# Kernel tuning notes

Measured on AMD Instinct MI355X. Metric: run time of the kernel, lower is better.

The kernel has to match this reference:

```python
import jax, jax.numpy as jnp
import numpy as np


def setup_inputs() -> dict:
    key = jax.random.key(0)
    k1, k2 = jax.random.split(key)
    batch, n = 1024, 32768
    x = jax.random.normal(k1, (batch, 1, n), dtype=jnp.float32)
    activ = jax.random.uniform(k2, (1, n), dtype=jnp.float32)  # EMA buffer state (nonnegative like mean(|x|))
    std = jnp.ones((1,), dtype=jnp.float32)
    return {"x": x, "activ": activ, "std": std}


def reference(x, activ, std):
    batch = x.shape[0]
    # EMA buffer update: activ = 0.97*activ + 0.03*mean(|x|, axis=0)
    activ_new = 0.97 * activ + 0.03 * jnp.mean(jnp.abs(x), axis=0)  # [1, n]
    ac = jnp.exp(-5.0 * jnp.squeeze(activ_new))                      # [n]
    s = jnp.sum(ac)
    ac = ac.at[0].set(s * 4000.0)  # heavily weight index 0 (the "no perturbation" slot)
    # torch.multinomial(ac, batch, replacement=True) == categorical with logits=log(weights)
    r = jax.random.categorical(jax.random.key(42), jnp.log(ac), shape=(batch,))  # [batch] in [0, n)
    i = jnp.arange(batch)
    # x[i, 0, r] += std * (r > 0); (i, r_i) pairs are unique per row so scatter-add == indexed add
    x = x.at[i, 0, r].add(std * (r > 0).astype(x.dtype))
    return x
```

## Files before the change

kernel.cpp:

```cpp
#include <hip/hip_runtime.h>
#include <math.h>

#define NROWS 1024
#define NCOLS 32768
#define NC4   (NCOLS / 4)
#define KCAND 16
#define TH_BITS 0xFFFC0000u
#define T_GUARD 7.9e-5f

__device__ __forceinline__ void tf_round(unsigned &x0, unsigned &x1, int r) {
    x0 += x1;
    x1 = __builtin_rotateleft32(x1, r);
    x1 ^= x0;
}

__device__ __forceinline__ void threefry2x32_key0_42(unsigned &x0, unsigned &x1) {
    const unsigned k0 = 0u;
    const unsigned k1 = 42u;
    const unsigned k2 = 0x1BD11BDAu ^ k0 ^ k1;
    x0 += k0; x1 += k1;
    tf_round(x0, x1, 13); tf_round(x0, x1, 15); tf_round(x0, x1, 26); tf_round(x0, x1, 6);
    x0 += k1; x1 += k2 + 1u;
    tf_round(x0, x1, 17); tf_round(x0, x1, 29); tf_round(x0, x1, 16); tf_round(x0, x1, 24);
    x0 += k2; x1 += k0 + 2u;
    tf_round(x0, x1, 13); tf_round(x0, x1, 15); tf_round(x0, x1, 26); tf_round(x0, x1, 6);
    x0 += k0; x1 += k1 + 3u;
    tf_round(x0, x1, 17); tf_round(x0, x1, 29); tf_round(x0, x1, 16); tf_round(x0, x1, 24);
    x0 += k1; x1 += k2 + 4u;
    tf_round(x0, x1, 13); tf_round(x0, x1, 15); tf_round(x0, x1, 26); tf_round(x0, x1, 6);
    x0 += k2; x1 += k0 + 5u;
}

__device__ __forceinline__ float bits_to_u(unsigned bits) {
    float u = __uint_as_float((bits >> 9) | 0x3f800000u) - 1.0f;
    return fmaxf(u, 1.17549435e-38f);
}

__global__ __launch_bounds__(256) void kF(
        const float4* __restrict__ x4, float4* __restrict__ out4,
        float4* __restrict__ partial4, unsigned* __restrict__ bits0,
        unsigned* __restrict__ cnt, uint2* __restrict__ cand, int nrb) {
    const int b = blockIdx.x;
    const int t = threadIdx.x;
    const int rpb = NROWS / nrb;

    auto copy_part = [&]() {
        if (b >= nrb * 32) return;
        const int bx = b & 31, by = b >> 5;
        const int j4 = bx * 256 + t;
        size_t base = (size_t)(by * rpb) * NC4 + j4;
        float4 acc = make_float4(0.f, 0.f, 0.f, 0.f);
        #pragma unroll 8
        for (int r = 0; r < rpb; ++r) {
            float4 v = x4[base];
            out4[base] = v;
            acc.x += fabsf(v.x); acc.y += fabsf(v.y);
            acc.z += fabsf(v.z); acc.w += fabsf(v.w);
            base += NC4;
        }
        partial4[(size_t)by * NC4 + j4] = acc;
    };

    auto scan_part = [&]() {
        const unsigned cbase = (unsigned)b * (unsigned)NCOLS;
        #pragma unroll 2
        for (int i = 0; i < NCOLS / 256; ++i) {
            const int j = t + (i << 8);
            unsigned x0 = 0u, x1 = cbase + (unsigned)j;
            threefry2x32_key0_42(x0, x1);
            const unsigned bits = x0 ^ x1;
            if (j == 0) {
                bits0[b] = bits;
            } else if (bits >= TH_BITS) {
                unsigned pos = atomicAdd(&cnt[b], 1u);
                if (pos < KCAND) cand[b * KCAND + pos] = make_uint2((unsigned)j, bits);
            }
        }
    };

    if (b & 1) { scan_part(); copy_part(); }
    else       { copy_part(); scan_part(); }
}

__global__ __launch_bounds__(256) void k2_weights(
        const float* __restrict__ partial, const float* __restrict__ activ,
        float* __restrict__ w, float* __restrict__ blocksums,
        float* __restrict__ blockmins, int nrb) {
    const int t = threadIdx.x;
    const int j = blockIdx.x * 256 + t;
    float s = 0.f;
    for (int rb = 0; rb < nrb; ++rb) s += partial[rb * NCOLS + j];
    float m  = s * (1.0f / (float)NROWS);
    float a  = 0.97f * activ[j] + 0.03f * m;
    float ac = expf(-5.0f * a);
    float wj = 1.0f / ac;
    w[j] = wj;
    __shared__ float reds[256];
    __shared__ float redm[256];
    reds[t] = ac;
    redm[t] = (j == 0) ? INFINITY : wj;
    __syncthreads();
    for (int off = 128; off > 0; off >>= 1) {
        if (t < off) {
            reds[t] += reds[t + off];
            redm[t] = fminf(redm[t], redm[t + off]);
        }
        __syncthreads();
    }
    if (t == 0) { blocksums[blockIdx.x] = reds[0]; blockmins[blockIdx.x] = redm[0]; }
}

__global__ __launch_bounds__(128) void k3_scalars(
        const float* __restrict__ blocksums, const float* __restrict__ blockmins,
        float* __restrict__ w, float* __restrict__ wminp) {
    const int t = threadIdx.x;
    __shared__ float reds[128];
    __shared__ float redm[128];
    reds[t] = blocksums[t];
    redm[t] = blockmins[t];
    __syncthreads();
    for (int off = 64; off > 0; off >>= 1) {
        if (t < off) {
            reds[t] += reds[t + off];
            redm[t] = fminf(redm[t], redm[t + off]);
        }
        __syncthreads();
    }
    if (t == 0) { w[0] = 1.0f / (reds[0] * 4000.0f); wminp[0] = redm[0]; }
}

__global__ __launch_bounds__(64) void k4b_resolve(
        const float* __restrict__ w, const unsigned* __restrict__ bits0,
        const unsigned* __restrict__ cnt, const uint2* __restrict__ cand,
        const float* __restrict__ wminp, const float* __restrict__ stdp,
        float* __restrict__ out) {
    const int r = blockIdx.x;
    const int t = threadIdx.x;
    const float w0   = w[0];
    const float wmin = wminp[0];
    const float val0 = -__log2f(bits_to_u(bits0[r])) * w0;
    const unsigned c = cnt[r];
    const bool slow = (c > KCAND) || !(val0 < T_GUARD * wmin);

    if (!slow) {
        if (t == 0 && c > 0) {
            float best = INFINITY;
            int   bi   = 0x7FFFFFFF;
            for (int k = 0; k < (int)c; ++k) {
                uint2 cd = cand[r * KCAND + k];
                float v = -__log2f(bits_to_u(cd.y)) * w[cd.x];
                int   j = (int)cd.x;
                if (v < best || (v == best && j < bi)) { best = v; bi = j; }
            }
            if (best < val0 && bi > 0 && bi < NCOLS)
                out[(size_t)r * NCOLS + bi] += stdp[0];
        }
        return;
    }

    const unsigned cbase = (unsigned)r * (unsigned)NCOLS;
    float best = INFINITY;
    int   bi   = 0x7FFFFFFF;
    for (int j = t; j < NCOLS; j += 64) {
        if (j == 0) continue;
        unsigned x0 = 0u, x1 = cbase + (unsigned)j;
        threefry2x32_key0_42(x0, x1);
        float v = -__log2f(bits_to_u(x0 ^ x1)) * w[j];
        if (v < best) { best = v; bi = j; }
    }
    __shared__ float sv[64];
    __shared__ int   si[64];
    sv[t] = best; si[t] = bi;
    __syncthreads();
    for (int off = 32; off > 0; off >>= 1) {
        if (t < off) {
            float ov = sv[t + off]; int oi = si[t + off];
            if (ov < sv[t] || (ov == sv[t] && oi < si[t])) { sv[t] = ov; si[t] = oi; }
        }
        __syncthreads();
    }
    if (t == 0) {
        if (sv[0] < val0 && si[0] > 0 && si[0] < NCOLS)
            out[(size_t)r * NCOLS + si[0]] += stdp[0];
    }
}

extern "C" void kernel_launch(void* const* d_in, const int* in_sizes, int n_in,
                              void* d_out, int out_size, void* d_ws, size_t ws_size,
                              hipStream_t stream) {
    (void)in_sizes; (void)n_in; (void)out_size;
    const float* x     = (const float*)d_in[0];
    const float* activ = (const float*)d_in[1];
    const float* stdp  = (const float*)d_in[2];
    float* out = (float*)d_out;
    char*  ws  = (char*)d_ws;

    const size_t tail_bytes = (size_t)NCOLS * 4 + 128 * 4 + 128 * 4 + 4
                            + NROWS * 4 + NROWS * 4 + (size_t)NROWS * KCAND * 8;
    int nrb = 16;
    if (ws_size >= (size_t)32 * NCOLS * 4 + tail_bytes) nrb = 32;

    float*    partial   = (float*)ws;
    float*    wbuf      = (float*)(ws + (size_t)nrb * NCOLS * 4);
    float*    blocksums = wbuf + NCOLS;
    float*    blockmins = blocksums + 128;
    float*    wminp     = blockmins + 128;
    unsigned* bits0     = (unsigned*)(wminp + 1);
    unsigned* cnt       = bits0 + NROWS;
    uint2*    cand      = (uint2*)(cnt + NROWS);

    hipMemsetAsync(cnt, 0, NROWS * sizeof(unsigned), stream);
    kF<<<NROWS, 256, 0, stream>>>((const float4*)x, (float4*)out,
                                  (float4*)partial, bits0, cnt, cand, nrb);
    k2_weights<<<NCOLS / 256, 256, 0, stream>>>(partial, activ, wbuf,
                                                blocksums, blockmins, nrb);
    k3_scalars<<<1, 128, 0, stream>>>(blocksums, blockmins, wbuf, wminp);
    k4b_resolve<<<NROWS, 64, 0, stream>>>(wbuf, bits0, cnt, cand, wminp,
                                          stdp, out);
}
```

Measured before the change: 303.0 us.

## Split copy and RNG scan into separate interleaved blocks; fold scalar reduction into resolve

The fused kernel no longer runs a copy and a full-row RNG scan in every block. Copy blocks are now interleaved with dedicated scan blocks, and each scan block covers half a row, giving 2048 scan blocks. The output copy uses nontemporal stores, and the candidate counters are zeroed inside the kernel, which removes the memset. The separate scalar-reduction kernel is dropped and its reduction is redone redundantly in each resolve block. This cuts two launches and should balance memory-bound and ALU-bound work across CUs, at the cost of extra redundant reductions and more total blocks.

```diff
diff --git a/kernel.cpp b/kernel.cpp
--- a/kernel.cpp
+++ b/kernel.cpp
@@ -4,9 +4,13 @@
 #define NROWS 1024
 #define NCOLS 32768
 #define NC4   (NCOLS / 4)
+#define HCOLS (NCOLS / 2)
+#define NB_SCAN 2048
 #define KCAND 16
 #define TH_BITS 0xFFFC0000u
 #define T_GUARD 7.9e-5f
+
+typedef float vfloat4 __attribute__((ext_vector_type(4)));
 
 __device__ __forceinline__ void tf_round(unsigned &x0, unsigned &x1, int r) {
     x0 += x1;
@@ -39,47 +43,49 @@
 __global__ __launch_bounds__(256) void kF(
         const float4* __restrict__ x4, float4* __restrict__ out4,
         float4* __restrict__ partial4, unsigned* __restrict__ bits0,
-        unsigned* __restrict__ cnt, uint2* __restrict__ cand, int nrb) {
+        unsigned* __restrict__ cnt, uint2* __restrict__ cand,
+        int nrb, int stride) {
     const int b = blockIdx.x;
     const int t = threadIdx.x;
-    const int rpb = NROWS / nrb;
-
-    auto copy_part = [&]() {
-        if (b >= nrb * 32) return;
-        const int bx = b & 31, by = b >> 5;
+
+    if (b % stride == 0) {
+        const int cid = b / stride;
+        const int rpb = NROWS / nrb;
+        const int bx = cid & 31, by = cid >> 5;
         const int j4 = bx * 256 + t;
         size_t base = (size_t)(by * rpb) * NC4 + j4;
         float4 acc = make_float4(0.f, 0.f, 0.f, 0.f);
         #pragma unroll 8
         for (int r = 0; r < rpb; ++r) {
             float4 v = x4[base];
-            out4[base] = v;
+            vfloat4 nv = { v.x, v.y, v.z, v.w };
+            __builtin_nontemporal_store(nv, (vfloat4*)&out4[base]);
             acc.x += fabsf(v.x); acc.y += fabsf(v.y);
             acc.z += fabsf(v.z); acc.w += fabsf(v.w);
             base += NC4;
         }
         partial4[(size_t)by * NC4 + j4] = acc;
-    };
-
-    auto scan_part = [&]() {
-        const unsigned cbase = (unsigned)b * (unsigned)NCOLS;
+    } else {
+        const int sid = b - b / stride - 1;
+        const int row = sid >> 1, half = sid & 1;
+        if (t == 0) cnt[sid] = 0;
+        __syncthreads();
+        const unsigned cbase = (unsigned)row * (unsigned)NCOLS;
+        const int jbase = half * HCOLS;
         #pragma unroll 2
-        for (int i = 0; i < NCOLS / 256; ++i) {
-            const int j = t + (i << 8);
+        for (int i = 0; i < HCOLS / 256; ++i) {
+            const int j = jbase + (i << 8) + t;
             unsigned x0 = 0u, x1 = cbase + (unsigned)j;
             threefry2x32_key0_42(x0, x1);
             const unsigned bits = x0 ^ x1;
             if (j == 0) {
-                bits0[b] = bits;
+                bits0[row] = bits;
             } else if (bits >= TH_BITS) {
-                unsigned pos = atomicAdd(&cnt[b], 1u);
-                if (pos < KCAND) cand[b * KCAND + pos] = make_uint2((unsigned)j, bits);
+                unsigned pos = atomicAdd(&cnt[sid], 1u);
+                if (pos < KCAND) cand[sid * KCAND + pos] = make_uint2((unsigned)j, bits);
             }
         }
-    };
-
-    if (b & 1) { scan_part(); copy_part(); }
-    else       { copy_part(); scan_part(); }
+    }
 }
 
 __global__ __launch_bounds__(256) void k2_weights(
@@ -110,44 +116,47 @@
     if (t == 0) { blocksums[blockIdx.x] = reds[0]; blockmins[blockIdx.x] = redm[0]; }
 }
 
-__global__ __launch_bounds__(128) void k3_scalars(
-        const float* __restrict__ blocksums, const float* __restrict__ blockmins,
-        float* __restrict__ w, float* __restrict__ wminp) {
-    const int t = threadIdx.x;
-    __shared__ float reds[128];
-    __shared__ float redm[128];
-    reds[t] = blocksums[t];
-    redm[t] = blockmins[t];
-    __syncthreads();
-    for (int off = 64; off > 0; off >>= 1) {
-        if (t < off) {
-            reds[t] += reds[t + off];
-            redm[t] = fminf(redm[t], redm[t + off]);
-        }
-        __syncthreads();
-    }
-    if (t == 0) { w[0] = 1.0f / (reds[0] * 4000.0f); wminp[0] = redm[0]; }
-}
-
-__global__ __launch_bounds__(64) void k4b_resolve(
-        const float* __restrict__ w, const unsigned* __restrict__ bits0,
+__global__ __launch_bounds__(64) void k4_resolve(
+        const float* __restrict__ w, const float* __restrict__ blocksums,
+        const float* __restrict__ blockmins, const unsigned* __restrict__ bits0,
         const unsigned* __restrict__ cnt, const uint2* __restrict__ cand,
-        const float* __restrict__ wminp, const float* __restrict__ stdp,
-        float* __restrict__ out) {
+        const float* __restrict__ stdp, float* __restrict__ out) {
     const int r = blockIdx.x;
     const int t = threadIdx.x;
-    const float w0   = w[0];
-    const float wmin = wminp[0];
+    __shared__ float sv[64];
+    __shared__ float sm[64];
+    __shared__ int   si[64];
+
+    sv[t] = blocksums[t] + blocksums[t + 64];
+    sm[t] = fminf(blockmins[t], blockmins[t + 64]);
+    __syncthreads();
+    for (int off = 32; off > 0; off >>= 1) {
+        if (t < off) {
+            sv[t] += sv[t + off];
+            sm[t] = fminf(sm[t], sm[t + off]);
+        }
+        __syncthreads();
+    }
+    const float w0   = 1.0f / (sv[0] * 4000.0f);
+    const float wmin = sm[0];
+
     const float val0 = -__log2f(bits_to_u(bits0[r])) * w0;
-    const unsigned c = cnt[r];
-    const bool slow = (c > KCAND) || !(val0 < T_GUARD * wmin);
+    const unsigned c0 = cnt[2 * r];
+    const unsigned c1 = cnt[2 * r + 1];
+    const bool slow = (c0 > KCAND) || (c1 > KCAND) || !(val0 < T_GUARD * wmin);
 
     if (!slow) {
-        if (t == 0 && c > 0) {
+        if (t == 0 && (c0 | c1) != 0u) {
             float best = INFINITY;
             int   bi   = 0x7FFFFFFF;
-            for (int k = 0; k < (int)c; ++k) {
-                uint2 cd = cand[r * KCAND + k];
+            for (int k = 0; k < (int)c0; ++k) {
+                uint2 cd = cand[(2 * r) * KCAND + k];
+                float v = -__log2f(bits_to_u(cd.y)) * w[cd.x];
+                int   j = (int)cd.x;
+                if (v < best || (v == best && j < bi)) { best = v; bi = j; }
+            }
+            for (int k = 0; k < (int)c1; ++k) {
+                uint2 cd = cand[(2 * r + 1) * KCAND + k];
                 float v = -__log2f(bits_to_u(cd.y)) * w[cd.x];
                 int   j = (int)cd.x;
                 if (v < best || (v == best && j < bi)) { best = v; bi = j; }
@@ -168,8 +177,7 @@
         float v = -__log2f(bits_to_u(x0 ^ x1)) * w[j];
         if (v < best) { best = v; bi = j; }
     }
-    __shared__ float sv[64];
-    __shared__ int   si[64];
+    __syncthreads();
     sv[t] = best; si[t] = bi;
     __syncthreads();
     for (int off = 32; off > 0; off >>= 1) {
@@ -195,8 +203,9 @@
     float* out = (float*)d_out;
     char*  ws  = (char*)d_ws;
 
-    const size_t tail_bytes = (size_t)NCOLS * 4 + 128 * 4 + 128 * 4 + 4
-                            + NROWS * 4 + NROWS * 4 + (size_t)NROWS * KCAND * 8;
+    const size_t tail_bytes = (size_t)NCOLS * 4 + 128 * 4 + 128 * 4
+                            + NROWS * 4 + (size_t)NB_SCAN * 4
+                            + (size_t)NB_SCAN * KCAND * 8;
     int nrb = 16;
     if (ws_size >= (size_t)32 * NCOLS * 4 + tail_bytes) nrb = 32;
 
@@ -204,17 +213,18 @@
     float*    wbuf      = (float*)(ws + (size_t)nrb * NCOLS * 4);
     float*    blocksums = wbuf + NCOLS;
     float*    blockmins = blocksums + 128;
-    float*    wminp     = blockmins + 128;
-    unsigned* bits0     = (unsigned*)(wminp + 1);
+    unsigned* bits0     = (unsigned*)(blockmins + 128);
     unsigned* cnt       = bits0 + NROWS;
-    uint2*    cand      = (uint2*)(cnt + NROWS);
-
-    hipMemsetAsync(cnt, 0, NROWS * sizeof(unsigned), stream);
-    kF<<<NROWS, 256, 0, stream>>>((const float4*)x, (float4*)out,
-                                  (float4*)partial, bits0, cnt, cand, nrb);
+    uint2*    cand      = (uint2*)(cnt + NB_SCAN);
+
+    const int ncopy  = nrb * 32;
+    const int stride = (ncopy + NB_SCAN) / ncopy;
+
+    kF<<<ncopy + NB_SCAN, 256, 0, stream>>>((const float4*)x, (float4*)out,
+                                            (float4*)partial, bits0, cnt, cand,
+                                            nrb, stride);
     k2_weights<<<NCOLS / 256, 256, 0, stream>>>(partial, activ, wbuf,
                                                 blocksums, blockmins, nrb);
-    k3_scalars<<<1, 128, 0, stream>>>(blocksums, blockmins, wbuf, wminp);
-    k4b_resolve<<<NROWS, 64, 0, stream>>>(wbuf, bits0, cnt, cand, wminp,
-                                          stdp, out);
-}
+    k4_resolve<<<NROWS, 64, 0, stream>>>(wbuf, blocksums, blockmins, bits0,
+                                         cnt, cand, stdp, out);
+}
```

Result: faster. 280.3 us (-7.5%).
